# Kernel optimization log

Hardware: AMD Instinct MI355X
Metric: run time of the kernel (lower is better)

The kernel has to match this reference:

```python
import jax, jax.numpy as jnp
import numpy as np

B, H, W, C = 16, 56, 56, 512
NH = 16
WS = 7
SHIFT = 3
HIDDEN = int(C * 4.0)
N = WS * WS
EPS = 1e-5


def _window_partition(x):
    # x: [B, H, W, C] -> [B*nW, N, C]
    b, h, w, c = x.shape
    x = x.reshape(b, h // WS, WS, w // WS, WS, c).transpose(0, 1, 3, 2, 4, 5)
    return x.reshape(-1, N, c)


def _window_reverse(win, h, w):
    c = win.shape[-1]
    x = win.reshape(-1, h // WS, w // WS, WS, WS, c).transpose(0, 1, 3, 2, 4, 5)
    return x.reshape(-1, h, w, c)


def _layernorm(x, g, b):
    mu = jnp.mean(x, axis=-1, keepdims=True)
    var = jnp.mean(jnp.square(x - mu), axis=-1, keepdims=True)
    return (x - mu) * jax.lax.rsqrt(var + EPS) * g + b


def _make_rel_coords_table():
    ch = np.arange(-(WS - 1), WS)
    cw = np.arange(-(WS - 1), WS)
    t = np.expand_dims(np.transpose(np.stack(np.meshgrid(ch, cw, indexing='ij')), [1, 2, 0]), 0).astype(np.float64)
    t[..., 0] /= (WS - 1)
    t[..., 1] /= (WS - 1)
    t *= 8
    t = np.sign(t) * np.log2(np.abs(t) + 1.0) / np.log2(8)
    return jnp.asarray(t, jnp.float32)  # [1, 2WS-1, 2WS-1, 2]


def _make_rel_pos_index():
    ch = np.arange(WS)
    cw = np.arange(WS)
    coords = np.reshape(np.stack(np.meshgrid(ch, cw, indexing='ij')), [2, -1])
    rel = np.expand_dims(coords, -1) - np.expand_dims(coords, -2)
    rel = np.transpose(rel, [1, 2, 0])
    rel[..., 0] += WS - 1
    rel[..., 1] += WS - 1
    rel[..., 0] *= 2 * WS - 1
    return jnp.asarray(np.sum(rel, -1), jnp.int32)  # [N, N]


def _make_attn_mask():
    img = np.zeros((H, W), np.float32)
    cnt = 0
    for hs in (slice(0, -WS), slice(-WS, -SHIFT), slice(-SHIFT, None)):
        for ws_ in (slice(0, -WS), slice(-WS, -SHIFT), slice(-SHIFT, None)):
            img[hs, ws_] = cnt
            cnt += 1
    x = img.reshape(1, H // WS, WS, W // WS, WS, 1).transpose(0, 1, 3, 2, 4, 5).reshape(-1, N)
    diff = x[:, :, None] - x[:, None, :]
    return jnp.asarray(np.where(diff != 0, -100.0, 0.0).astype(np.float32))  # [nW, N, N]


def setup_inputs() -> dict:
    key = jax.random.key(0)
    ks = jax.random.split(key, 16)
    s = 0.02
    return {
        'x': jax.random.normal(ks[0], (B, H, W, C), jnp.float32),
        'qkv_w': jax.random.normal(ks[1], (C, 3 * C), jnp.float32) * s,
        'q_bias': jnp.zeros((C,), jnp.float32),
        'v_bias': jnp.zeros((C,), jnp.float32),
        'proj_w': jax.random.normal(ks[2], (C, C), jnp.float32) * s,
        'proj_b': jnp.zeros((C,), jnp.float32),
        'logit_scale': jnp.full((NH, 1, 1), np.log(10.0), jnp.float32),
        'cpb_w1': jax.random.normal(ks[3], (2, 512), jnp.float32) * s,
        'cpb_b1': jnp.zeros((512,), jnp.float32),
        'cpb_w2': jax.random.normal(ks[4], (512, NH), jnp.float32) * s,
        'rel_coords_table': _make_rel_coords_table(),
        'gamma1': jnp.ones((C,), jnp.float32),
        'beta1': jnp.zeros((C,), jnp.float32),
        'gamma2': jnp.ones((C,), jnp.float32),
        'beta2': jnp.zeros((C,), jnp.float32),
        'fc1_w': jax.random.normal(ks[5], (C, HIDDEN), jnp.float32) * s,
        'fc1_b': jnp.zeros((HIDDEN,), jnp.float32),
        'fc2_w': jax.random.normal(ks[6], (HIDDEN, C), jnp.float32) * s,
        'fc2_b': jnp.zeros((C,), jnp.float32),
        'rel_pos_index': _make_rel_pos_index(),
        'attn_mask': _make_attn_mask(),
    }


def _forward(x, qkv_w, q_bias, v_bias, proj_w, proj_b, logit_scale,
             cpb_w1, cpb_b1, cpb_w2, rel_coords_table,
             gamma1, beta1, gamma2, beta2, fc1_w, fc1_b, fc2_w, fc2_b,
             rel_pos_index, attn_mask):
    hd = C // NH
    shortcut = x
    # cyclic shift + window partition
    xs = jnp.roll(x, (-SHIFT, -SHIFT), axis=(1, 2))
    xw = _window_partition(xs)  # [B*nW, N, C]
    # qkv with (q, 0, v) bias
    qkv_bias = jnp.concatenate([q_bias, jnp.zeros_like(v_bias), v_bias], axis=0)
    qkv = xw @ qkv_w + qkv_bias
    qkv = qkv.reshape(-1, N, 3, NH, hd).transpose(2, 0, 3, 1, 4)
    q, k, v = qkv[0], qkv[1], qkv[2]  # [BW, NH, N, hd]
    # cosine attention with learned temperature
    qn = q / jnp.linalg.norm(q, axis=-1, keepdims=True)
    kn = k / jnp.linalg.norm(k, axis=-1, keepdims=True)
    scale = jnp.exp(jnp.minimum(logit_scale, jnp.log(100.0)))
    attn = jnp.einsum('bhnd,bhmd->bhnm', qn, kn) * scale
    # continuous position bias via small MLP + gather
    cpb = jax.nn.relu(rel_coords_table @ cpb_w1 + cpb_b1) @ cpb_w2  # [1,2W-1,2W-1,NH]
    table = cpb.reshape(-1, NH)
    bias = table[rel_pos_index.reshape(-1)].reshape(N, N, NH).transpose(2, 0, 1)
    bias = 16.0 * jax.nn.sigmoid(bias)
    attn = attn + bias[None]
    # shifted-window mask
    nW = attn_mask.shape[0]
    attn = attn.reshape(-1, nW, NH, N, N) + attn_mask[None, :, None]
    attn = jax.nn.softmax(attn.reshape(-1, NH, N, N), axis=-1)
    out = jnp.einsum('bhnm,bhmd->bhnd', attn, v).transpose(0, 2, 1, 3).reshape(-1, N, C)
    out = out @ proj_w + proj_b
    # reverse windows + reverse shift
    out = _window_reverse(out, H, W)
    out = jnp.roll(out, (SHIFT, SHIFT), axis=(1, 2))
    # Swin-V2 res-post-norm residual blocks
    x1 = shortcut + _layernorm(out, gamma1, beta1)
    h = jax.nn.gelu(x1 @ fc1_w + fc1_b, approximate=False) @ fc2_w + fc2_b
    return x1 + _layernorm(h, gamma2, beta2)


def reference(x, qkv_w, q_bias, v_bias, proj_w, proj_b, logit_scale,
              cpb_w1, cpb_b1, cpb_w2, rel_coords_table,
              gamma1, beta1, gamma2, beta2, fc1_w, fc1_b, fc2_w, fc2_b,
              rel_pos_index, attn_mask):
    return _forward(x, qkv_w, q_bias, v_bias, proj_w, proj_b, logit_scale,
                    cpb_w1, cpb_b1, cpb_w2, rel_coords_table,
                    gamma1, beta1, gamma2, beta2, fc1_w, fc1_b, fc2_w, fc2_b,
                    rel_pos_index, attn_mask)
```

## Files before the change

kernel.cpp:

```cpp
#include <hip/hip_runtime.h>
#include <hip/hip_bf16.h>
#include <cmath>

typedef __hip_bfloat16 bf16;
typedef __attribute__((ext_vector_type(8))) __bf16 bf16x8;
typedef __attribute__((ext_vector_type(4))) float f32x4;
typedef __attribute__((ext_vector_type(4))) short short4v;

#define NROWS 50176

static __device__ __forceinline__ float b2f(bf16 v) { return __bfloat162float(v); }
static __device__ __forceinline__ bf16 f2b(float v) { return __float2bfloat16(v); }

static __device__ __forceinline__ size_t pix_base(int row) {
  if (row >= NROWS) row = NROWS - 1;
  int win = row / 49, tok = row - win * 49;
  int b = win >> 6, wi = win & 63;
  int th = tok / 7, tw = tok - th * 7;
  int h = (wi >> 3) * 7 + th + 3; if (h >= 56) h -= 56;
  int w = (wi & 7) * 7 + tw + 3;  if (w >= 56) w -= 56;
  return (((size_t)b * 56 + h) * 56 + w) * 512;
}

__global__ __launch_bounds__(256) void diag_fill(float* out, float val, int n) {
  int i = blockIdx.x * 256 + threadIdx.x;
  if (i < n) out[i] = val;
}

__global__ __launch_bounds__(256) void transpose_f2b(const float* __restrict__ in,
                                                     bf16* __restrict__ out,
                                                     int R, int C) {
  __shared__ float tile[32][33];
  int c0 = blockIdx.x * 32, r0 = blockIdx.y * 32;
  int tx = threadIdx.x & 31, ty = threadIdx.x >> 5;
  for (int i = ty; i < 32; i += 8)
    tile[i][tx] = in[(size_t)(r0 + i) * C + c0 + tx];
  __syncthreads();
  for (int i = ty; i < 32; i += 8)
    out[(size_t)(c0 + i) * R + r0 + tx] = f2b(tile[tx][i]);
}

__global__ void prep_small(const float* qb, const float* vb, const float* pb,
                           const float* f1b, const float* f2b_, const float* ls,
                           float* qkvb, float* pbf, float* f1bf, float* f2bf,
                           float* scale) {
  int tid = blockIdx.x * 256 + threadIdx.x;
  if (tid < 512)       qkvb[tid] = qb[tid];
  else if (tid < 1024) qkvb[tid] = 0.f;
  else if (tid < 1536) qkvb[tid] = vb[tid - 1024];
  if (tid < 512)  pbf[tid]  = pb[tid];
  if (tid < 2048) f1bf[tid] = f1b[tid];
  if (tid < 512)  f2bf[tid] = f2b_[tid];
  if (tid < 16)   scale[tid] = expf(fminf(ls[tid], 4.6051701859880914f));
}

__global__ __launch_bounds__(256) void prep_cpb(const float* __restrict__ coords,
                                                const float* __restrict__ w1,
                                                const float* __restrict__ b1,
                                                const float* __restrict__ w2,
                                                float* __restrict__ table) {
  __shared__ float hid[512];
  __shared__ float part[256];
  int idx = blockIdx.x;
  float c0 = coords[idx * 2], c1 = coords[idx * 2 + 1];
  int tid = threadIdx.x;
  for (int h = tid; h < 512; h += 256) {
    float v = c0 * w1[h] + c1 * w1[512 + h] + b1[h];
    hid[h] = fmaxf(v, 0.f);
  }
  __syncthreads();
  int head = tid & 15, seg = tid >> 4;
  float s = 0.f;
  for (int h = seg * 32; h < seg * 32 + 32; ++h) s += hid[h] * w2[h * 16 + head];
  part[tid] = s;
  __syncthreads();
  if (tid < 16) {
    float t = 0.f;
    for (int sg = 0; sg < 16; ++sg) t += part[sg * 16 + tid];
    table[idx * 16 + tid] = t;
  }
}

__global__ void prep_bias(const float* __restrict__ table, const int* __restrict__ rpi,
                          float* __restrict__ bias_full) {
  int idx = blockIdx.x * 256 + threadIdx.x;
  if (idx >= 16 * 2401) return;
  int head = idx / 2401, ij = idx - head * 2401;
  float t = table[rpi[ij] * 16 + head];
  bias_full[idx] = 16.f / (1.f + expf(-t));
}

__global__ void prep_bm(const float* __restrict__ biasF, const float* __restrict__ amask,
                        float* __restrict__ bm) {
  int idx = blockIdx.x * 256 + threadIdx.x;
  if (idx >= 64 * 16 * 2401) return;
  int w = idx / (16 * 2401);
  int rem = idx - w * (16 * 2401);
  int h = rem / 2401, ij = rem - h * 2401;
  bm[idx] = biasF[h * 2401 + ij] + amask[w * 2401 + ij];
}

template <int EPI, int AF32>
__global__ __launch_bounds__(256, 2) void gemm_kernel(const void* Aq, int lda,
                                                      const bf16* __restrict__ Bt,
                                                      bf16* C, int ldc,
                                                      const float* __restrict__ bias,
                                                      int K) {
  constexpr int LP = 40;
  __shared__ __align__(16) bf16 As[128 * LP];
  __shared__ __align__(16) bf16 Bs[128 * LP];
  const int tid = threadIdx.x;
  const int lane = tid & 63;
  const int quad = lane >> 4;
  const int l15 = lane & 15;
  const int wave = tid >> 6;
  const int wm = (wave >> 1) * 64;
  const int wn = (wave & 1) * 64;
  const int row0 = blockIdx.y * 128;
  const int col0 = blockIdx.x * 128;
  const int r0 = tid >> 2, kc = (tid & 3) << 3;

  f32x4 acc[4][4] = {};

  for (int k0 = 0; k0 < K; k0 += 32) {
    if (AF32) {
      const float* A = (const float*)Aq;
#pragma unroll
      for (int half = 0; half < 2; ++half) {
        size_t off = (size_t)(row0 + r0 + half * 64) * lda + k0 + kc;
        float4 u0 = *(const float4*)&A[off];
        float4 u1 = *(const float4*)&A[off + 4];
        bf16 h8[8] = {f2b(u0.x), f2b(u0.y), f2b(u0.z), f2b(u0.w),
                      f2b(u1.x), f2b(u1.y), f2b(u1.z), f2b(u1.w)};
        *(uint4*)&As[(r0 + half * 64) * LP + kc] = *(uint4*)h8;
      }
    } else {
      const bf16* A = (const bf16*)Aq;
      *(uint4*)&As[r0 * LP + kc]        = *(const uint4*)&A[(size_t)(row0 + r0) * lda + k0 + kc];
      *(uint4*)&As[(r0 + 64) * LP + kc] = *(const uint4*)&A[(size_t)(row0 + r0 + 64) * lda + k0 + kc];
    }
    *(uint4*)&Bs[r0 * LP + kc]        = *(const uint4*)&Bt[(size_t)(col0 + r0) * K + k0 + kc];
    *(uint4*)&Bs[(r0 + 64) * LP + kc] = *(const uint4*)&Bt[(size_t)(col0 + r0 + 64) * K + k0 + kc];
    __syncthreads();
    bf16x8 af[4], bfr[4];
#pragma unroll
    for (int t = 0; t < 4; ++t) {
      af[t]  = *(const bf16x8*)&As[(wm + t * 16 + l15) * LP + quad * 8];
      bfr[t] = *(const bf16x8*)&Bs[(wn + t * 16 + l15) * LP + quad * 8];
    }
#pragma unroll
    for (int mt = 0; mt < 4; ++mt)
#pragma unroll
      for (int nt = 0; nt < 4; ++nt)
        acc[mt][nt] = __builtin_amdgcn_mfma_f32_16x16x32_bf16(af[mt], bfr[nt], acc[mt][nt], 0, 0, 0);
    __syncthreads();
  }

#pragma unroll
  for (int nt = 0; nt < 4; ++nt) {
    int gcol = col0 + wn + nt * 16 + l15;
    float bv = bias[gcol];
#pragma unroll
    for (int mt = 0; mt < 4; ++mt) {
      int grow = row0 + wm + mt * 16 + quad * 4;
#pragma unroll
      for (int r = 0; r < 4; ++r) {
        float v = acc[mt][nt][r] + bv;
        if (EPI == 2) v = 0.5f * v * (1.0f + erff(v * 0.70710678118654752f));
        C[(size_t)(grow + r) * ldc + gcol] = f2b(v);
      }
    }
  }
}

__global__ __launch_bounds__(256, 2) void gemm_qkv(const float* __restrict__ X,
                                                   const bf16* __restrict__ Bt,
                                                   bf16* __restrict__ C,
                                                   const float* __restrict__ bias,
                                                   int row_off) {
  constexpr int LP = 40;
  constexpr int K = 512;
  __shared__ __align__(16) bf16 As[128 * LP];
  __shared__ __align__(16) bf16 Bs[128 * LP];
  const int tid = threadIdx.x;
  const int lane = tid & 63;
  const int quad = lane >> 4;
  const int l15 = lane & 15;
  const int wave = tid >> 6;
  const int wm = (wave >> 1) * 64;
  const int wn = (wave & 1) * 64;
  const int row0 = blockIdx.y * 128;
  const int col0 = blockIdx.x * 128;
  const int r0 = tid >> 2, kc = (tid & 3) << 3;
  const size_t base0 = pix_base(row_off + row0 + r0);
  const size_t base1 = pix_base(row_off + row0 + r0 + 64);

  f32x4 acc[4][4] = {};

  for (int k0 = 0; k0 < K; k0 += 32) {
    {
      float4 u0 = *(const float4*)&X[base0 + k0 + kc];
      float4 u1 = *(const float4*)&X[base0 + k0 + kc + 4];
      bf16 h8[8] = {f2b(u0.x), f2b(u0.y), f2b(u0.z), f2b(u0.w),
                    f2b(u1.x), f2b(u1.y), f2b(u1.z), f2b(u1.w)};
      *(uint4*)&As[r0 * LP + kc] = *(uint4*)h8;
      float4 v0 = *(const float4*)&X[base1 + k0 + kc];
      float4 v1 = *(const float4*)&X[base1 + k0 + kc + 4];
      bf16 g8[8] = {f2b(v0.x), f2b(v0.y), f2b(v0.z), f2b(v0.w),
                    f2b(v1.x), f2b(v1.y), f2b(v1.z), f2b(v1.w)};
      *(uint4*)&As[(r0 + 64) * LP + kc] = *(uint4*)g8;
    }
    *(uint4*)&Bs[r0 * LP + kc]        = *(const uint4*)&Bt[(size_t)(col0 + r0) * K + k0 + kc];
    *(uint4*)&Bs[(r0 + 64) * LP + kc] = *(const uint4*)&Bt[(size_t)(col0 + r0 + 64) * K + k0 + kc];
    __syncthreads();
    bf16x8 af[4], bfr[4];
#pragma unroll
    for (int t = 0; t < 4; ++t) {
      af[t]  = *(const bf16x8*)&As[(wm + t * 16 + l15) * LP + quad * 8];
      bfr[t] = *(const bf16x8*)&Bs[(wn + t * 16 + l15) * LP + quad * 8];
    }
#pragma unroll
    for (int mt = 0; mt < 4; ++mt)
#pragma unroll
      for (int nt = 0; nt < 4; ++nt)
        acc[mt][nt] = __builtin_amdgcn_mfma_f32_16x16x32_bf16(af[mt], bfr[nt], acc[mt][nt], 0, 0, 0);
    __syncthreads();
  }

#pragma unroll
  for (int nt = 0; nt < 4; ++nt) {
    int gcol = col0 + wn + nt * 16 + l15;
    float bv = bias[gcol];
#pragma unroll
    for (int mt = 0; mt < 4; ++mt) {
      int grow = row0 + wm + mt * 16 + quad * 4;
#pragma unroll
      for (int r = 0; r < 4; ++r)
        C[(size_t)(grow + r) * 1536 + gcol] = f2b(acc[mt][nt][r] + bv);
    }
  }
}

__global__ __launch_bounds__(256, 4) void attn_mfma(const bf16* __restrict__ qkv,
                                                    const float* __restrict__ scale,
                                                    const float* __restrict__ bm,
                                                    bf16* __restrict__ outp, int win_off) {
  __shared__ __align__(16) __bf16 Vl[4][1984];
  const int tid = threadIdx.x;
  const int wave = tid >> 6, lane = tid & 63;
  const int quad = lane >> 4, l15 = lane & 15;
  const int winl = blockIdx.x >> 2, hg = blockIdx.x & 3;
  const int head = hg * 4 + wave;
  const int wing = win_off + winl;
  const size_t rowbase = (size_t)winl * 49;
  const __bf16* base = (const __bf16*)qkv + rowbase * 1536 + head * 32;
  __bf16* Vw = Vl[wave];
  const float* bmh = bm + ((size_t)(wing & 63) * 16 + head) * 2401;
  const float sc = scale[head];

  bf16x8 vtmp[4];
  int vj[4], vdc[4];
#pragma unroll
  for (int t = 0; t < 4; ++t) {
    int c = lane + 64 * t; if (c > 195) c = 195;
    vj[t] = c >> 2; vdc[t] = (c & 3) << 3;
    vtmp[t] = *(const bf16x8*)(base + (size_t)vj[t] * 1536 + 1024 + vdc[t]);
  }

  bf16x8 khi[4], klo[4];
#pragma unroll
  for (int jt = 0; jt < 4; ++jt) {
    int j = jt * 16 + l15; if (j > 48) j = 48;
    bf16x8 raw = *(const bf16x8*)(base + (size_t)j * 1536 + 512 + quad * 8);
    float f[8]; float ss = 1e-20f;
#pragma unroll
    for (int e = 0; e < 8; ++e) { f[e] = (float)raw[e]; ss += f[e] * f[e]; }
    ss += __shfl_xor(ss, 16, 64);
    ss += __shfl_xor(ss, 32, 64);
    float inv = rsqrtf(ss);
#pragma unroll
    for (int e = 0; e < 8; ++e) {
      float v = f[e] * inv;
      __bf16 h = (__bf16)v;
      khi[jt][e] = h;
      klo[jt][e] = (__bf16)(v - (float)h);
    }
  }

#pragma unroll
  for (int t = 0; t < 4; ++t)
    *(bf16x8*)&Vw[vj[t] * 40 + vdc[t]] = vtmp[t];

  short4v vb[4][2];
#pragma unroll
  for (int jt = 0; jt < 4; ++jt)
#pragma unroll
    for (int n2 = 0; n2 < 2; ++n2) {
      short4v v;
#pragma unroll
      for (int e = 0; e < 4; ++e) {
        int j = jt * 16 + quad * 4 + e; if (j > 48) j = 48;
        v[e] = *(const short*)&Vw[j * 40 + n2 * 16 + l15];
      }
      vb[jt][n2] = v;
    }

  for (int it = 0; it < 4; ++it) {
    int qi = it * 16 + l15; if (qi > 48) qi = 48;
    bf16x8 raw = *(const bf16x8*)(base + (size_t)qi * 1536 + quad * 8);
    float f[8]; float ss = 1e-20f;
#pragma unroll
    for (int e = 0; e < 8; ++e) { f[e] = (float)raw[e]; ss += f[e] * f[e]; }
    ss += __shfl_xor(ss, 16, 64);
    ss += __shfl_xor(ss, 32, 64);
    float qinv = rsqrtf(ss) * sc;
    bf16x8 qhi, qlo;
#pragma unroll
    for (int e = 0; e < 8; ++e) {
      float v = f[e] * qinv;
      __bf16 h = (__bf16)v;
      qhi[e] = h;
      qlo[e] = (__bf16)(v - (float)h);
    }
    f32x4 s4[4];
#pragma unroll
    for (int jt = 0; jt < 4; ++jt) {
      f32x4 a = {0.f, 0.f, 0.f, 0.f};
      a = __builtin_amdgcn_mfma_f32_16x16x32_bf16(khi[jt], qhi, a, 0, 0, 0);
      a = __builtin_amdgcn_mfma_f32_16x16x32_bf16(klo[jt], qhi, a, 0, 0, 0);
      a = __builtin_amdgcn_mfma_f32_16x16x32_bf16(khi[jt], qlo, a, 0, 0, 0);
      s4[jt] = a;
    }
    int iio = (qi) * 49;
    float sv[4][4];
    float mx = -1e30f;
#pragma unroll
    for (int jt = 0; jt < 4; ++jt)
#pragma unroll
      for (int r = 0; r < 4; ++r) {
        int j = jt * 16 + quad * 4 + r;
        float s = (j < 49) ? s4[jt][r] + bmh[iio + j] : -1e30f;
        sv[jt][r] = s;
        mx = fmaxf(mx, s);
      }
    mx = fmaxf(mx, __shfl_xor(mx, 16, 64));
    mx = fmaxf(mx, __shfl_xor(mx, 32, 64));
    float sum = 0.f;
#pragma unroll
    for (int jt = 0; jt < 4; ++jt)
#pragma unroll
      for (int r = 0; r < 4; ++r) {
        float e = exp2f((sv[jt][r] - mx) * 1.4426950408889634f);
        sv[jt][r] = e;
        sum += e;
      }
    sum += __shfl_xor(sum, 16, 64);
    sum += __shfl_xor(sum, 32, 64);
    float pinv = 1.f / sum;
    short4v pa[4];
#pragma unroll
    for (int jt = 0; jt < 4; ++jt)
#pragma unroll
      for (int r = 0; r < 4; ++r) {
        __bf16 h = (__bf16)(sv[jt][r] * pinv);
        pa[jt][r] = *(short*)&h;
      }
    f32x4 o[2] = {};
#pragma unroll
    for (int jt = 0; jt < 4; ++jt) {
#pragma unroll
      for (int n2 = 0; n2 < 2; ++n2)
        o[n2] = __builtin_amdgcn_mfma_f32_16x16x16bf16_1k(pa[jt], vb[jt][n2], o[n2], 0, 0, 0);
    }
#pragma unroll
    for (int n2 = 0; n2 < 2; ++n2)
#pragma unroll
      for (int r = 0; r < 4; ++r) {
        int i = it * 16 + quad * 4 + r;
        if (i < 49)
          outp[(rowbase + i) * 1536 + head * 32 + n2 * 16 + l15] = f2b(o[n2][r]);
      }
  }
}

__global__ __launch_bounds__(256) void ln_shift_add(const bf16* projq,
                                                    const float* __restrict__ x,
                                                    const float* __restrict__ gamma,
                                                    const float* __restrict__ beta,
                                                    float* __restrict__ x1,
                                                    int row_off) {
  __shared__ float red[10];
  int grow = row_off + blockIdx.x;
  int win = grow / 49, tok = grow - win * 49;
  int b = win >> 6, wi = win & 63;
  int hs = (wi >> 3) * 7 + tok / 7;
  int wsc = (wi & 7) * 7 + tok % 7;
  int h = hs + 3; if (h >= 56) h -= 56;
  int w = wsc + 3; if (w >= 56) w -= 56;
  size_t pix = ((size_t)b * 56 + h) * 56 + w;
  const bf16* src = projq + (size_t)blockIdx.x * 1536 + 512;
  int tid = threadIdx.x;
  float a0 = b2f(src[tid]);
  float a1 = b2f(src[tid + 256]);
  float s = a0 + a1, q = a0 * a0 + a1 * a1;
#pragma unroll
  for (int off = 32; off > 0; off >>= 1) {
    s += __shfl_down(s, off, 64);
    q += __shfl_down(q, off, 64);
  }
  int lane = tid & 63, wv = tid >> 6;
  if (lane == 0) { red[wv] = s; red[4 + wv] = q; }
  __syncthreads();
  if (tid == 0) {
    red[8] = red[0] + red[1] + red[2] + red[3];
    red[9] = red[4] + red[5] + red[6] + red[7];
  }
  __syncthreads();
  float mu = red[8] * (1.f / 512.f);
  float inv = rsqrtf(fmaxf(red[9] * (1.f / 512.f) - mu * mu, 0.f) + 1e-5f);
  size_t base = pix * 512;
  x1[base + tid]       = x[base + tid]       + (a0 - mu) * inv * gamma[tid]       + beta[tid];
  x1[base + tid + 256] = x[base + tid + 256] + (a1 - mu) * inv * gamma[tid + 256] + beta[tid + 256];
}

__global__ __launch_bounds__(256) void ln_add(const bf16* __restrict__ hsrc,
                                              float* x1,
                                              const float* __restrict__ gamma,
                                              const float* __restrict__ beta) {
  __shared__ float red[10];
  size_t base = (size_t)blockIdx.x * 512;
  int tid = threadIdx.x;
  float a0 = b2f(hsrc[base + tid]);
  float a1 = b2f(hsrc[base + tid + 256]);
  float s = a0 + a1, q = a0 * a0 + a1 * a1;
#pragma unroll
  for (int off = 32; off > 0; off >>= 1) {
    s += __shfl_down(s, off, 64);
    q += __shfl_down(q, off, 64);
  }
  int lane = tid & 63, wv = tid >> 6;
  if (lane == 0) { red[wv] = s; red[4 + wv] = q; }
  __syncthreads();
  if (tid == 0) {
    red[8] = red[0] + red[1] + red[2] + red[3];
    red[9] = red[4] + red[5] + red[6] + red[7];
  }
  __syncthreads();
  float mu = red[8] * (1.f / 512.f);
  float inv = rsqrtf(fmaxf(red[9] * (1.f / 512.f) - mu * mu, 0.f) + 1e-5f);
  x1[base + tid]       += (a0 - mu) * inv * gamma[tid]       + beta[tid];
  x1[base + tid + 256] += (a1 - mu) * inv * gamma[tid + 256] + beta[tid + 256];
}

extern "C" void kernel_launch(void* const* d_in, const int* in_sizes, int n_in,
                              void* d_out, int out_size, void* d_ws, size_t ws_size,
                              hipStream_t stream) {
  const float* x       = (const float*)d_in[0];
  const float* qkv_w   = (const float*)d_in[1];
  const float* q_bias  = (const float*)d_in[2];
  const float* v_bias  = (const float*)d_in[3];
  const float* proj_w  = (const float*)d_in[4];
  const float* proj_b  = (const float*)d_in[5];
  const float* logit_s = (const float*)d_in[6];
  const float* cpb_w1  = (const float*)d_in[7];
  const float* cpb_b1  = (const float*)d_in[8];
  const float* cpb_w2  = (const float*)d_in[9];
  const float* rct     = (const float*)d_in[10];
  const float* gamma1  = (const float*)d_in[11];
  const float* beta1   = (const float*)d_in[12];
  const float* gamma2  = (const float*)d_in[13];
  const float* beta2   = (const float*)d_in[14];
  const float* fc1_w   = (const float*)d_in[15];
  const float* fc1_b   = (const float*)d_in[16];
  const float* fc2_w   = (const float*)d_in[17];
  const float* fc2_b   = (const float*)d_in[18];
  const int*   rpi     = (const int*)d_in[19];
  const float* amask   = (const float*)d_in[20];
  float* out = (float*)d_out;

  char* ws = (char*)d_ws;
  size_t cur = 0;
  auto alloc = [&](size_t bytes) { size_t o = cur; cur += (bytes + 255) & ~(size_t)255; return o; };
  size_t o_qkvb = alloc(1536 * 4);
  size_t o_pb   = alloc(512 * 4);
  size_t o_f1b  = alloc(2048 * 4);
  size_t o_f2b  = alloc(512 * 4);
  size_t o_scal = alloc(16 * 4);
  size_t o_tab  = alloc(169 * 16 * 4);
  size_t o_bias = alloc(16 * 2401 * 4);
  size_t o_bm   = alloc((size_t)64 * 16 * 2401 * 4);
  size_t o_wt1  = alloc((size_t)1536 * 512 * 2);
  size_t o_wt2  = alloc((size_t)512 * 512 * 2);
  size_t o_wt3  = alloc((size_t)2048 * 512 * 2);
  size_t o_wt4  = alloc((size_t)512 * 2048 * 2);
  size_t o_big  = cur;
  size_t avail  = (ws_size > o_big) ? ws_size - o_big : 0;

  const int wopts[] = {1024, 256, 128, 64, 32, 16, 8};
  int wA = 0, padA = 0;
  for (int i = 0; i < 7; ++i) {
    int rows = wopts[i] * 49;
    int pad = (rows + 127) & ~127;
    if ((size_t)pad * 1536 * 2 <= avail) { wA = wopts[i]; padA = pad; break; }
  }
  const int ropts[] = {25088, 12544, 6272, 3584, 1792, 896, 512, 256};
  int rB = 0;
  for (int i = 0; i < 8; ++i)
    if ((size_t)ropts[i] * 2560 * 2 <= avail) { rB = ropts[i]; break; }

  if (!wA || !rB) {
    float v = 20000.f + (float)(ws_size >> 20);
    diag_fill<<<(out_size + 255) / 256, 256, 0, stream>>>(out, v, out_size);
    return;
  }

  float* qkvb  = (float*)(ws + o_qkvb);
  float* pbf   = (float*)(ws + o_pb);
  float* f1bf  = (float*)(ws + o_f1b);
  float* f2bf  = (float*)(ws + o_f2b);
  float* scal  = (float*)(ws + o_scal);
  float* tab   = (float*)(ws + o_tab);
  float* biasF = (float*)(ws + o_bias);
  float* bmF   = (float*)(ws + o_bm);
  bf16* wt1 = (bf16*)(ws + o_wt1);
  bf16* wt2 = (bf16*)(ws + o_wt2);
  bf16* wt3 = (bf16*)(ws + o_wt3);
  bf16* wt4 = (bf16*)(ws + o_wt4);
  bf16* big = (bf16*)(ws + o_big);

  transpose_f2b<<<dim3(48, 16), 256, 0, stream>>>(qkv_w, wt1, 512, 1536);
  transpose_f2b<<<dim3(16, 16), 256, 0, stream>>>(proj_w, wt2, 512, 512);
  transpose_f2b<<<dim3(64, 16), 256, 0, stream>>>(fc1_w, wt3, 512, 2048);
  transpose_f2b<<<dim3(16, 64), 256, 0, stream>>>(fc2_w, wt4, 2048, 512);

  prep_small<<<8, 256, 0, stream>>>(q_bias, v_bias, proj_b, fc1_b, fc2_b, logit_s,
                                    qkvb, pbf, f1bf, f2bf, scal);
  prep_cpb<<<169, 256, 0, stream>>>(rct, cpb_w1, cpb_b1, cpb_w2, tab);
  prep_bias<<<151, 256, 0, stream>>>(tab, rpi, biasF);
  prep_bm<<<(64 * 16 * 2401 + 255) / 256, 256, 0, stream>>>(biasF, amask, bmF);

  for (int woff = 0; woff < 1024; woff += wA) {
    int row_off = woff * 49;
    int rows = wA * 49;
    bf16* qkvC = big;
    gemm_qkv<<<dim3(12, padA / 128), 256, 0, stream>>>(x, wt1, qkvC, qkvb, row_off);
    attn_mfma<<<wA * 4, 256, 0, stream>>>(qkvC, scal, bmF, qkvC, woff);
    gemm_kernel<1, 0><<<dim3(4, padA / 128), 256, 0, stream>>>(qkvC, 1536, wt2, qkvC + 512, 1536, pbf, 512);
    ln_shift_add<<<rows, 256, 0, stream>>>(qkvC, x, gamma1, beta1, out, row_off);
  }
  for (int r0 = 0; r0 < NROWS; r0 += rB) {
    float* x1h = out + (size_t)r0 * 512;
    bf16* hC  = big;
    bf16* f2C = big + (size_t)rB * 2048;
    gemm_kernel<2, 1><<<dim3(16, rB / 128), 256, 0, stream>>>(x1h, 512, wt3, hC, 2048, f1bf, 512);
    gemm_kernel<1, 0><<<dim3(4, rB / 128), 256, 0, stream>>>(hC, 2048, wt4, f2C, 512, f2bf, 2048);
    ln_add<<<rB, 256, 0, stream>>>(f2C, x1h, gamma2, beta2);
  }
}
```

Baseline: 1.074 ms.

## Use direct global-to-LDS loads with swizzle and XCD remap in GEMMs

```diff
diff --git a/kernel.cpp b/kernel.cpp
--- a/kernel.cpp
+++ b/kernel.cpp
@@ -11,6 +11,11 @@
 
 static __device__ __forceinline__ float b2f(bf16 v) { return __bfloat162float(v); }
 static __device__ __forceinline__ bf16 f2b(float v) { return __float2bfloat16(v); }
+
+static __device__ __forceinline__ void gl16(const bf16* g, bf16* l) {
+  __builtin_amdgcn_global_load_lds((const __attribute__((address_space(1))) void*)g,
+                                   (__attribute__((address_space(3))) void*)l, 16, 0, 0);
+}
 
 static __device__ __forceinline__ size_t pix_base(int row) {
   if (row >= NROWS) row = NROWS - 1;
@@ -38,6 +43,17 @@
   __syncthreads();
   for (int i = ty; i < 32; i += 8)
     out[(size_t)(c0 + i) * R + r0 + tx] = f2b(tile[tx][i]);
+}
+
+__global__ __launch_bounds__(256) void conv_f2b(const float* __restrict__ in,
+                                                bf16* __restrict__ outb, int n8) {
+  for (int i = blockIdx.x * 256 + threadIdx.x; i < n8; i += gridDim.x * 256) {
+    float4 u0 = *(const float4*)&in[(size_t)i * 8];
+    float4 u1 = *(const float4*)&in[(size_t)i * 8 + 4];
+    bf16 h8[8] = {f2b(u0.x), f2b(u0.y), f2b(u0.z), f2b(u0.w),
+                  f2b(u1.x), f2b(u1.y), f2b(u1.z), f2b(u1.w)};
+    *(uint4*)&outb[(size_t)i * 8] = *(uint4*)h8;
+  }
 }
 
 __global__ void prep_small(const float* qb, const float* vb, const float* pb,
@@ -100,53 +116,62 @@
   bm[idx] = biasF[h * 2401 + ij] + amask[w * 2401 + ij];
 }
 
-template <int EPI, int AF32>
-__global__ __launch_bounds__(256, 2) void gemm_kernel(const void* Aq, int lda,
-                                                      const bf16* __restrict__ Bt,
-                                                      bf16* C, int ldc,
-                                                      const float* __restrict__ bias,
-                                                      int K) {
-  constexpr int LP = 40;
-  __shared__ __align__(16) bf16 As[128 * LP];
-  __shared__ __align__(16) bf16 Bs[128 * LP];
+template <int EPI, int GATHER>
+__global__ __launch_bounds__(256, 4) void gemm_lds(const bf16* __restrict__ A, int lda,
+                                                   const bf16* __restrict__ Bt,
+                                                   bf16* __restrict__ C, int ldc,
+                                                   const float* __restrict__ bias,
+                                                   int K, int nbx, int row_off) {
+  __shared__ __align__(16) bf16 As[128 * 32];
+  __shared__ __align__(16) bf16 Bs[128 * 32];
+  const int nwg = gridDim.x, bid = blockIdx.x;
+  const int q = nwg >> 3, r = nwg & 7;
+  const int xcd = bid & 7, coff = bid >> 3;
+  const int wg = (xcd < r ? xcd * (q + 1) : r * (q + 1) + (xcd - r) * q) + coff;
+  const int bx = wg % nbx, by = wg / nbx;
+  const int row0 = by * 128, col0 = bx * 128;
+
   const int tid = threadIdx.x;
   const int lane = tid & 63;
-  const int quad = lane >> 4;
-  const int l15 = lane & 15;
+  const int quad = lane >> 4, l15 = lane & 15;
   const int wave = tid >> 6;
-  const int wm = (wave >> 1) * 64;
-  const int wn = (wave & 1) * 64;
-  const int row0 = blockIdx.y * 128;
-  const int col0 = blockIdx.x * 128;
-  const int r0 = tid >> 2, kc = (tid & 3) << 3;
+  const int wm = (wave >> 1) * 64, wn = (wave & 1) * 64;
+  const int xq = quad ^ ((l15 >> 1) & 3);
+
+  const int ar0 = tid >> 2, as0 = tid & 3;
+  const int ar1 = ar0 + 64;
+  const int ax0 = as0 ^ ((ar0 >> 1) & 3);
+  const int ax1 = as0 ^ ((ar1 >> 1) & 3);
+  size_t ab0, ab1;
+  if (GATHER) {
+    ab0 = pix_base(row_off + row0 + ar0);
+    ab1 = pix_base(row_off + row0 + ar1);
+  } else {
+    ab0 = (size_t)(row0 + ar0) * lda;
+    ab1 = (size_t)(row0 + ar1) * lda;
+  }
+  const bf16* ap0 = A + ab0 + ax0 * 8;
+  const bf16* ap1 = A + ab1 + ax1 * 8;
+  const bf16* bp0 = Bt + (size_t)(col0 + ar0) * K + ax0 * 8;
+  const bf16* bp1 = Bt + (size_t)(col0 + ar1) * K + ax1 * 8;
+  bf16* la0 = As + tid * 8;
+  bf16* la1 = As + (tid + 256) * 8;
+  bf16* lb0 = Bs + tid * 8;
+  bf16* lb1 = Bs + (tid + 256) * 8;
 
   f32x4 acc[4][4] = {};
 
   for (int k0 = 0; k0 < K; k0 += 32) {
-    if (AF32) {
-      const float* A = (const float*)Aq;
-#pragma unroll
-      for (int half = 0; half < 2; ++half) {
-        size_t off = (size_t)(row0 + r0 + half * 64) * lda + k0 + kc;
-        float4 u0 = *(const float4*)&A[off];
-        float4 u1 = *(const float4*)&A[off + 4];
-        bf16 h8[8] = {f2b(u0.x), f2b(u0.y), f2b(u0.z), f2b(u0.w),
-                      f2b(u1.x), f2b(u1.y), f2b(u1.z), f2b(u1.w)};
-        *(uint4*)&As[(r0 + half * 64) * LP + kc] = *(uint4*)h8;
-      }
-    } else {
-      const bf16* A = (const bf16*)Aq;
-      *(uint4*)&As[r0 * LP + kc]        = *(const uint4*)&A[(size_t)(row0 + r0) * lda + k0 + kc];
-      *(uint4*)&As[(r0 + 64) * LP + kc] = *(const uint4*)&A[(size_t)(row0 + r0 + 64) * lda + k0 + kc];
-    }
-    *(uint4*)&Bs[r0 * LP + kc]        = *(const uint4*)&Bt[(size_t)(col0 + r0) * K + k0 + kc];
-    *(uint4*)&Bs[(r0 + 64) * LP + kc] = *(const uint4*)&Bt[(size_t)(col0 + r0 + 64) * K + k0 + kc];
+    gl16(ap0 + k0, la0);
+    gl16(ap1 + k0, la1);
+    gl16(bp0 + k0, lb0);
+    gl16(bp1 + k0, lb1);
     __syncthreads();
     bf16x8 af[4], bfr[4];
 #pragma unroll
     for (int t = 0; t < 4; ++t) {
-      af[t]  = *(const bf16x8*)&As[(wm + t * 16 + l15) * LP + quad * 8];
-      bfr[t] = *(const bf16x8*)&Bs[(wn + t * 16 + l15) * LP + quad * 8];
+      af[t]  = *(const bf16x8*)&As[(wm + t * 16 + l15) * 32 + xq * 8];
+      bfr[t] = *(const bf16x8*)&Bs[(wn + t * 16 + l15) * 32 + xq * 8];
     }
 #pragma unroll
     for (int mt = 0; mt < 4; ++mt)
@@ -164,79 +189,11 @@
     for (int mt = 0; mt < 4; ++mt) {
       int grow = row0 + wm + mt * 16 + quad * 4;
 #pragma unroll
-      for (int r = 0; r < 4; ++r) {
-        float v = acc[mt][nt][r] + bv;
+      for (int rr = 0; rr < 4; ++rr) {
+        float v = acc[mt][nt][rr] + bv;
         if (EPI == 2) v = 0.5f * v * (1.0f + erff(v * 0.70710678118654752f));
-        C[(size_t)(grow + r) * ldc + gcol] = f2b(v);
+        C[(size_t)(grow + rr) * ldc + gcol] = f2b(v);
       }
-    }
-  }
-}
-
-__global__ __launch_bounds__(256, 2) void gemm_qkv(const float* __restrict__ X,
-                                                   const bf16* __restrict__ Bt,
-                                                   bf16* __restrict__ C,
-                                                   const float* __restrict__ bias,
-                                                   int row_off) {
-  constexpr int LP = 40;
-  constexpr int K = 512;
-  __shared__ __align__(16) bf16 As[128 * LP];
-  __shared__ __align__(16) bf16 Bs[128 * LP];
-  const int tid = threadIdx.x;
-  const int lane = tid & 63;
-  const int quad = lane >> 4;
-  const int l15 = lane & 15;
-  const int wave = tid >> 6;
-  const int wm = (wave >> 1) * 64;
-  const int wn = (wave & 1) * 64;
-  const int row0 = blockIdx.y * 128;
-  const int col0 = blockIdx.x * 128;
-  const int r0 = tid >> 2, kc = (tid & 3) << 3;
-  const size_t base0 = pix_base(row_off + row0 + r0);
-  const size_t base1 = pix_base(row_off + row0 + r0 + 64);
-
-  f32x4 acc[4][4] = {};
-
-  for (int k0 = 0; k0 < K; k0 += 32) {
-    {
-      float4 u0 = *(const float4*)&X[base0 + k0 + kc];
-      float4 u1 = *(const float4*)&X[base0 + k0 + kc + 4];
-      bf16 h8[8] = {f2b(u0.x), f2b(u0.y), f2b(u0.z), f2b(u0.w),
-                    f2b(u1.x), f2b(u1.y), f2b(u1.z), f2b(u1.w)};
-      *(uint4*)&As[r0 * LP + kc] = *(uint4*)h8;
-      float4 v0 = *(const float4*)&X[base1 + k0 + kc];
-      float4 v1 = *(const float4*)&X[base1 + k0 + kc + 4];
-      bf16 g8[8] = {f2b(v0.x), f2b(v0.y), f2b(v0.z), f2b(v0.w),
-                    f2b(v1.x), f2b(v1.y), f2b(v1.z), f2b(v1.w)};
-      *(uint4*)&As[(r0 + 64) * LP + kc] = *(uint4*)g8;
-    }
-    *(uint4*)&Bs[r0 * LP + kc]        = *(const uint4*)&Bt[(size_t)(col0 + r0) * K + k0 + kc];
-    *(uint4*)&Bs[(r0 + 64) * LP + kc] = *(const uint4*)&Bt[(size_t)(col0 + r0 + 64) * K + k0 + kc];
-    __syncthreads();
-    bf16x8 af[4], bfr[4];
-#pragma unroll
-    for (int t = 0; t < 4; ++t) {
-      af[t]  = *(const bf16x8*)&As[(wm + t * 16 + l15) * LP + quad * 8];
-      bfr[t] = *(const bf16x8*)&Bs[(wn + t * 16 + l15) * LP + quad * 8];
-    }
-#pragma unroll
-    for (int mt = 0; mt < 4; ++mt)
-#pragma unroll
-      for (int nt = 0; nt < 4; ++nt)
-        acc[mt][nt] = __builtin_amdgcn_mfma_f32_16x16x32_bf16(af[mt], bfr[nt], acc[mt][nt], 0, 0, 0);
-    __syncthreads();
-  }
-
-#pragma unroll
-  for (int nt = 0; nt < 4; ++nt) {
-    int gcol = col0 + wn + nt * 16 + l15;
-    float bv = bias[gcol];
-#pragma unroll
-    for (int mt = 0; mt < 4; ++mt) {
-      int grow = row0 + wm + mt * 16 + quad * 4;
-#pragma unroll
-      for (int r = 0; r < 4; ++r)
-        C[(size_t)(grow + r) * 1536 + gcol] = f2b(acc[mt][nt][r] + bv);
     }
   }
 }
@@ -331,16 +288,16 @@
       a = __builtin_amdgcn_mfma_f32_16x16x32_bf16(khi[jt], qlo, a, 0, 0, 0);
       s4[jt] = a;
     }
-    int iio = (qi) * 49;
+    int iio = qi * 49;
     float sv[4][4];
     float mx = -1e30f;
 #pragma unroll
     for (int jt = 0; jt < 4; ++jt)
 #pragma unroll
-      for (int r = 0; r < 4; ++r) {
-        int j = jt * 16 + quad * 4 + r;
-        float s = (j < 49) ? s4[jt][r] + bmh[iio + j] : -1e30f;
-        sv[jt][r] = s;
+      for (int rr = 0; rr < 4; ++rr) {
+        int j = jt * 16 + quad * 4 + rr;
+        float s = (j < 49) ? s4[jt][rr] + bmh[iio + j] : -1e30f;
+        sv[jt][rr] = s;
         mx = fmaxf(mx, s);
       }
     mx = fmaxf(mx, __shfl_xor(mx, 16, 64));
@@ -349,9 +306,9 @@
 #pragma unroll
     for (int jt = 0; jt < 4; ++jt)
 #pragma unroll
-      for (int r = 0; r < 4; ++r) {
-        float e = exp2f((sv[jt][r] - mx) * 1.4426950408889634f);
-        sv[jt][r] = e;
+      for (int rr = 0; rr < 4; ++rr) {
+        float e = exp2f((sv[jt][rr] - mx) * 1.4426950408889634f);
+        sv[jt][rr] = e;
         sum += e;
       }
     sum += __shfl_xor(sum, 16, 64);
@@ -361,9 +318,9 @@
 #pragma unroll
     for (int jt = 0; jt < 4; ++jt)
 #pragma unroll
-      for (int r = 0; r < 4; ++r) {
-        __bf16 h = (__bf16)(sv[jt][r] * pinv);
-        pa[jt][r] = *(short*)&h;
+      for (int rr = 0; rr < 4; ++rr) {
+        __bf16 h = (__bf16)(sv[jt][rr] * pinv);
+        pa[jt][rr] = *(short*)&h;
       }
     f32x4 o[2] = {};
 #pragma unroll
@@ -375,10 +332,10 @@
 #pragma unroll
     for (int n2 = 0; n2 < 2; ++n2)
 #pragma unroll
-      for (int r = 0; r < 4; ++r) {
-        int i = it * 16 + quad * 4 + r;
+      for (int rr = 0; rr < 4; ++rr) {
+        int i = it * 16 + quad * 4 + rr;
         if (i < 49)
-          outp[(rowbase + i) * 1536 + head * 32 + n2 * 16 + l15] = f2b(o[n2][r]);
+          outp[(rowbase + i) * 1536 + head * 32 + n2 * 16 + l15] = f2b(o[n2][rr]);
       }
   }
 }
@@ -388,6 +345,7 @@
                                                     const float* __restrict__ gamma,
                                                     const float* __restrict__ beta,
                                                     float* __restrict__ x1,
+                                                    bf16* __restrict__ x1b,
                                                     int row_off) {
   __shared__ float red[10];
   int grow = row_off + blockIdx.x;
@@ -402,14 +360,14 @@
   int tid = threadIdx.x;
   float a0 = b2f(src[tid]);
   float a1 = b2f(src[tid + 256]);
-  float s = a0 + a1, q = a0 * a0 + a1 * a1;
+  float s = a0 + a1, qq = a0 * a0 + a1 * a1;
 #pragma unroll
   for (int off = 32; off > 0; off >>= 1) {
     s += __shfl_down(s, off, 64);
-    q += __shfl_down(q, off, 64);
+    qq += __shfl_down(qq, off, 64);
   }
   int lane = tid & 63, wv = tid >> 6;
-  if (lane == 0) { red[wv] = s; red[4 + wv] = q; }
+  if (lane == 0) { red[wv] = s; red[4 + wv] = qq; }
   __syncthreads();
   if (tid == 0) {
     red[8] = red[0] + red[1] + red[2] + red[3];
@@ -419,8 +377,12 @@
   float mu = red[8] * (1.f / 512.f);
   float inv = rsqrtf(fmaxf(red[9] * (1.f / 512.f) - mu * mu, 0.f) + 1e-5f);
   size_t base = pix * 512;
-  x1[base + tid]       = x[base + tid]       + (a0 - mu) * inv * gamma[tid]       + beta[tid];
-  x1[base + tid + 256] = x[base + tid + 256] + (a1 - mu) * inv * gamma[tid + 256] + beta[tid + 256];
+  float v0 = x[base + tid]       + (a0 - mu) * inv * gamma[tid]       + beta[tid];
+  float v1 = x[base + tid + 256] + (a1 - mu) * inv * gamma[tid + 256] + beta[tid + 256];
+  x1[base + tid]        = v0;
+  x1[base + tid + 256]  = v1;
+  x1b[base + tid]       = f2b(v0);
+  x1b[base + tid + 256] = f2b(v1);
 }
 
 __global__ __launch_bounds__(256) void ln_add(const bf16* __restrict__ hsrc,
@@ -432,14 +394,14 @@
   int tid = threadIdx.x;
   float a0 = b2f(hsrc[base + tid]);
   float a1 = b2f(hsrc[base + tid + 256]);
-  float s = a0 + a1, q = a0 * a0 + a1 * a1;
+  float s = a0 + a1, qq = a0 * a0 + a1 * a1;
 #pragma unroll
   for (int off = 32; off > 0; off >>= 1) {
     s += __shfl_down(s, off, 64);
-    q += __shfl_down(q, off, 64);
+    qq += __shfl_down(qq, off, 64);
   }
   int lane = tid & 63, wv = tid >> 6;
-  if (lane == 0) { red[wv] = s; red[4 + wv] = q; }
+  if (lane == 0) { red[wv] = s; red[4 + wv] = qq; }
   __syncthreads();
   if (tid == 0) {
     red[8] = red[0] + red[1] + red[2] + red[3];
@@ -493,12 +455,14 @@
   size_t o_wt2  = alloc((size_t)512 * 512 * 2);
   size_t o_wt3  = alloc((size_t)2048 * 512 * 2);
   size_t o_wt4  = alloc((size_t)512 * 2048 * 2);
+  size_t o_xb   = alloc((size_t)NROWS * 512 * 2);
+  size_t o_x1b  = alloc((size_t)NROWS * 512 * 2);
   size_t o_big  = cur;
   size_t avail  = (ws_size > o_big) ? ws_size - o_big : 0;
 
-  const int wopts[] = {1024, 256, 128, 64, 32, 16, 8};
+  const int wopts[] = {1024, 512, 256, 128, 64, 32, 16, 8};
   int wA = 0, padA = 0;
-  for (int i = 0; i < 7; ++i) {
+  for (int i = 0; i < 8; ++i) {
     int rows = wopts[i] * 49;
     int pad = (rows + 127) & ~127;
     if ((size_t)pad * 1536 * 2 <= avail) { wA = wopts[i]; padA = pad; break; }
@@ -526,12 +490,15 @@
   bf16* wt2 = (bf16*)(ws + o_wt2);
   bf16* wt3 = (bf16*)(ws + o_wt3);
   bf16* wt4 = (bf16*)(ws + o_wt4);
+  bf16* xb  = (bf16*)(ws + o_xb);
+  bf16* x1b = (bf16*)(ws + o_x1b);
   bf16* big = (bf16*)(ws + o_big);
 
   transpose_f2b<<<dim3(48, 16), 256, 0, stream>>>(qkv_w, wt1, 512, 1536);
   transpose_f2b<<<dim3(16, 16), 256, 0, stream>>>(proj_w, wt2, 512, 512);
   transpose_f2b<<<dim3(64, 16), 256, 0, stream>>>(fc1_w, wt3, 512, 2048);
   transpose_f2b<<<dim3(16, 64), 256, 0, stream>>>(fc2_w, wt4, 2048, 512);
+  conv_f2b<<<2048, 256, 0, stream>>>(x, xb, NROWS * 512 / 8);
 
   prep_small<<<8, 256, 0, stream>>>(q_bias, v_bias, proj_b, fc1_b, fc2_b, logit_s,
                                     qkvb, pbf, f1bf, f2bf, scal);
@@ -542,18 +509,20 @@
   for (int woff = 0; woff < 1024; woff += wA) {
     int row_off = woff * 49;
     int rows = wA * 49;
+    int nby = padA / 128;
     bf16* qkvC = big;
-    gemm_qkv<<<dim3(12, padA / 128), 256, 0, stream>>>(x, wt1, qkvC, qkvb, row_off);
+    gemm_lds<1, 1><<<12 * nby, 256, 0, stream>>>(xb, 0, wt1, qkvC, 1536, qkvb, 512, 12, row_off);
     attn_mfma<<<wA * 4, 256, 0, stream>>>(qkvC, scal, bmF, qkvC, woff);
-    gemm_kernel<1, 0><<<dim3(4, padA / 128), 256, 0, stream>>>(qkvC, 1536, wt2, qkvC + 512, 1536, pbf, 512);
-    ln_shift_add<<<rows, 256, 0, stream>>>(qkvC, x, gamma1, beta1, out, row_off);
+    gemm_lds<1, 0><<<4 * nby, 256, 0, stream>>>(qkvC, 1536, wt2, qkvC + 512, 1536, pbf, 512, 4, 0);
+    ln_shift_add<<<rows, 256, 0, stream>>>(qkvC, x, gamma1, beta1, out, x1b, row_off);
   }
   for (int r0 = 0; r0 < NROWS; r0 += rB) {
     float* x1h = out + (size_t)r0 * 512;
     bf16* hC  = big;
     bf16* f2C = big + (size_t)rB * 2048;
-    gemm_kernel<2, 1><<<dim3(16, rB / 128), 256, 0, stream>>>(x1h, 512, wt3, hC, 2048, f1bf, 512);
-    gemm_kernel<1, 0><<<dim3(4, rB / 128), 256, 0, stream>>>(hC, 2048, wt4, f2C, 512, f2bf, 2048);
+    int nby = rB / 128;
+    gemm_lds<2, 0><<<16 * nby, 256, 0, stream>>>(x1b + (size_t)r0 * 512, 512, wt3, hC, 2048, f1bf, 512, 16, 0);
+    gemm_lds<1, 0><<<4 * nby, 256, 0, stream>>>(hC, 2048, wt4, f2C, 512, f2bf, 2048, 4, 0);
     ln_add<<<rB, 256, 0, stream>>>(f2C, x1h, gamma2, beta2);
   }
 }
```

After: 958.0 us. 1.12x faster.
